# Kernel optimization log

Measured on AMD Instinct MI355X. Metric: run time of the kernel, lower is better.

The kernel has to match this reference:

```python
import jax, jax.numpy as jnp
import numpy as np

N_NODES = 50000
N_EDGES = 400000
LAT = 128
NODE_F = 3
EDGE_F = 4
OUT = 3
STEPS = 5
EPS = 1e-5


def _ln_mlp(h, w1, b1, w2, b2, g, be):
    # Linear -> ReLU -> Linear -> ReLU -> LayerNorm
    h = jax.nn.relu(h @ w1 + b1)
    h = jax.nn.relu(h @ w2 + b2)
    mu = jnp.mean(h, axis=-1, keepdims=True)
    var = jnp.mean((h - mu) ** 2, axis=-1, keepdims=True)
    return (h - mu) * jax.lax.rsqrt(var + EPS) * g + be


def _mlp_p(key, din, d):
    k = jax.random.split(key, 2)
    s1 = 1.0 / np.sqrt(din)
    s2 = 1.0 / np.sqrt(d)
    return (jax.random.normal(k[0], (din, d), jnp.float32) * s1, jnp.zeros((d,), jnp.float32),
            jax.random.normal(k[1], (d, d), jnp.float32) * s2, jnp.zeros((d,), jnp.float32),
            jnp.ones((d,), jnp.float32), jnp.zeros((d,), jnp.float32))


def setup_inputs() -> dict:
    key = jax.random.key(0)
    ks = jax.random.split(key, 8)
    d = {
        "x": jax.random.normal(ks[0], (N_NODES, NODE_F), jnp.float32),
        "edge_attr": jax.random.normal(ks[1], (N_EDGES, EDGE_F), jnp.float32),
        "edge_index": jax.random.randint(ks[2], (2, N_EDGES), 0, N_NODES, jnp.int64 if jax.config.jax_enable_x64 else jnp.int32),
    }
    for pre, din, k in (("ne", NODE_F, ks[3]), ("ee", EDGE_F, ks[4]), ("em", 3 * LAT, ks[5]), ("nm", 2 * LAT, ks[6])):
        w1, b1, w2, b2, g, be = _mlp_p(k, din, LAT)
        d[pre + "_w1"] = w1; d[pre + "_b1"] = b1
        d[pre + "_w2"] = w2; d[pre + "_b2"] = b2
        d[pre + "_g"] = g; d[pre + "_be"] = be
    kd = jax.random.split(ks[7], 2)
    d["dec_w1"] = jax.random.normal(kd[0], (LAT, LAT), jnp.float32) / np.sqrt(LAT)
    d["dec_b1"] = jnp.zeros((LAT,), jnp.float32)
    d["dec_w2"] = jax.random.normal(kd[1], (LAT, OUT), jnp.float32) / np.sqrt(LAT)
    d["dec_b2"] = jnp.zeros((OUT,), jnp.float32)
    return d


def reference(x, edge_attr, edge_index,
              ne_w1, ne_b1, ne_w2, ne_b2, ne_g, ne_be,
              ee_w1, ee_b1, ee_w2, ee_b2, ee_g, ee_be,
              em_w1, em_b1, em_w2, em_b2, em_g, em_be,
              nm_w1, nm_b1, nm_w2, nm_b2, nm_g, nm_be,
              dec_w1, dec_b1, dec_w2, dec_b2):
    n = x.shape[0]
    src, dst = edge_index[0], edge_index[1]  # PyG: edge_index[0]=source(j), [1]=target(i)

    h = _ln_mlp(x, ne_w1, ne_b1, ne_w2, ne_b2, ne_g, ne_be)          # [N, LAT]
    e = _ln_mlp(edge_attr, ee_w1, ee_b1, ee_w2, ee_b2, ee_g, ee_be)   # [E, LAT]

    for _ in range(STEPS):  # shared-weight GraphNetBlock applied STEPS times
        # message: cat([x_i, x_j, e]) = cat([h[dst], h[src], e]), aggregated at dst
        msg = _ln_mlp(jnp.concatenate([h[dst], h[src], e], axis=-1),
                      em_w1, em_b1, em_w2, em_b2, em_g, em_be)
        agg = jax.ops.segment_sum(msg, dst, num_segments=n)           # [N, LAT]
        h_new = _ln_mlp(jnp.concatenate([agg, h], axis=-1),
                        nm_w1, nm_b1, nm_w2, nm_b2, nm_g, nm_be) + h
        # new edge features use cat([x[row], x[col], e]) = cat([h[src], h[dst], e])
        e = _ln_mlp(jnp.concatenate([h[src], h[dst], e], axis=-1),
                    em_w1, em_b1, em_w2, em_b2, em_g, em_be) + e
        h = h_new

    return jax.nn.relu(h @ dec_w1 + dec_b1) @ dec_w2 + dec_b2         # [N, OUT]
```

## Files before the change

### kernel.cpp

```cpp
#include <hip/hip_runtime.h>

#define LAT 128
#define LATP 132
#define EPS 1e-5f
#define EB 32
#define TS 136

typedef __attribute__((ext_vector_type(8))) short bs8;
typedef __attribute__((ext_vector_type(4))) float fx4;

__device__ __forceinline__ float bf2f(unsigned int u) {
    return __uint_as_float(u << 16);
}
__device__ __forceinline__ unsigned short f2bf(float f) {
    unsigned int x = __float_as_uint(f);
    x += 0x7fffu + ((x >> 16) & 1u);
    return (unsigned short)(x >> 16);
}
__device__ __forceinline__ void unpack8(uint4 u, float* v) {
    v[0] = bf2f(u.x & 0xffffu); v[1] = bf2f(u.x >> 16);
    v[2] = bf2f(u.y & 0xffffu); v[3] = bf2f(u.y >> 16);
    v[4] = bf2f(u.z & 0xffffu); v[5] = bf2f(u.z >> 16);
    v[6] = bf2f(u.w & 0xffffu); v[7] = bf2f(u.w >> 16);
}
__device__ __forceinline__ uint4 pack8(const float* v) {
    uint4 u;
    u.x = (unsigned)f2bf(v[0]) | ((unsigned)f2bf(v[1]) << 16);
    u.y = (unsigned)f2bf(v[2]) | ((unsigned)f2bf(v[3]) << 16);
    u.z = (unsigned)f2bf(v[4]) | ((unsigned)f2bf(v[5]) << 16);
    u.w = (unsigned)f2bf(v[6]) | ((unsigned)f2bf(v[7]) << 16);
    return u;
}
__device__ __forceinline__ bs8 cvt8(const float* p) {
    bs8 r;
    #pragma unroll
    for (int i = 0; i < 8; i++) r[i] = (short)f2bf(p[i]);
    return r;
}

__global__ __launch_bounds__(256) void zero_kernel(float4* __restrict__ p, int n4) {
    int i = blockIdx.x * 256 + threadIdx.x;
    if (i < n4) p[i] = make_float4(0.f, 0.f, 0.f, 0.f);
}

__global__ void probe_kernel(int* __restrict__ rowtab, int* __restrict__ coltab) {
    int l = threadIdx.x;
    bs8 idv, ones;
    unsigned short ridb = f2bf((float)(l & 15));
    unsigned short oneb = f2bf(1.f);
    #pragma unroll
    for (int i = 0; i < 8; i++) { idv[i] = (short)ridb; ones[i] = (short)oneb; }
    fx4 dR = {0.f, 0.f, 0.f, 0.f};
    fx4 dC = {0.f, 0.f, 0.f, 0.f};
    dR = __builtin_amdgcn_mfma_f32_16x16x32_bf16(idv, ones, dR, 0, 0, 0);
    dC = __builtin_amdgcn_mfma_f32_16x16x32_bf16(ones, idv, dC, 0, 0, 0);
    #pragma unroll
    for (int reg = 0; reg < 4; reg++) {
        rowtab[l * 4 + reg] = ((int)(dR[reg] * (1.f / 32.f) + 0.5f)) & 15;
        coltab[l * 4 + reg] = ((int)(dC[reg] * (1.f / 32.f) + 0.5f)) & 15;
    }
}

__global__ __launch_bounds__(256) void pack_w_kernel(
    const float* __restrict__ src, unsigned short* __restrict__ dst, int KS)
{
    int id = blockIdx.x * 256 + threadIdx.x;
    if (id >= KS * 4096) return;
    int j = id & 7;
    int l = (id >> 3) & 63;
    int rest = id >> 9;
    int ks = rest % KS, nt = rest / KS;
    int k = ks * 32 + (l >> 4) * 8 + j;
    int n = nt * 16 + (l & 15);
    dst[id] = f2bf(src[k * 128 + n]);
}

template<int KIN>
__global__ __launch_bounds__(256) void encode_kernel(
    const float* __restrict__ x, unsigned short* __restrict__ out,
    const float* __restrict__ w1, const float* __restrict__ b1,
    const float* __restrict__ w2, const float* __restrict__ b2,
    const float* __restrict__ gam, const float* __restrict__ bet, int M)
{
    __shared__ float l1[8][LAT];
    __shared__ float l2[8][LAT];
    const int t = threadIdx.x;
    const int base = blockIdx.x * 8;
    const int j = t & 127, g = t >> 7;

    float wv[KIN];
    #pragma unroll
    for (int u = 0; u < KIN; u++) wv[u] = w1[u * LAT + j];
    const float bb = b1[j];
    #pragma unroll
    for (int i = 0; i < 4; i++) {
        int e = g + 2 * i; int row = base + e;
        float acc = bb;
        if (row < M) {
            #pragma unroll
            for (int u = 0; u < KIN; u++) acc += x[(size_t)row * KIN + u] * wv[u];
        }
        l1[e][j] = fmaxf(acc, 0.f);
    }
    __syncthreads();

    float s2[4] = {0.f, 0.f, 0.f, 0.f};
    for (int k = 0; k < LAT; k += 4) {
        float w[4];
        #pragma unroll
        for (int u = 0; u < 4; u++) w[u] = w2[(k + u) * LAT + j];
        #pragma unroll
        for (int i = 0; i < 4; i++) {
            int e = g + 2 * i;
            float4 v4 = *(const float4*)&l1[e][k];
            s2[i] += v4.x * w[0] + v4.y * w[1] + v4.z * w[2] + v4.w * w[3];
        }
    }
    const float b2v = b2[j];
    #pragma unroll
    for (int i = 0; i < 4; i++) { int e = g + 2 * i; l2[e][j] = fmaxf(s2[i] + b2v, 0.f); }
    __syncthreads();

    const int wv_ = t >> 6, lane = t & 63;
    #pragma unroll
    for (int which = 0; which < 2; which++) {
        int e = 2 * wv_ + which; int row = base + e;
        if (row >= M) continue;
        float v0 = l2[e][lane], v1 = l2[e][lane + 64];
        float s1 = v0 + v1, sq = v0 * v0 + v1 * v1;
        #pragma unroll
        for (int m = 32; m >= 1; m >>= 1) { s1 += __shfl_xor(s1, m); sq += __shfl_xor(sq, m); }
        float mu = s1 * (1.f / LAT);
        float var = sq * (1.f / LAT) - mu * mu;
        float inv = rsqrtf(var + EPS);
        out[(size_t)row * LAT + lane]      = f2bf((v0 - mu) * inv * gam[lane]      + bet[lane]);
        out[(size_t)row * LAT + lane + 64] = f2bf((v1 - mu) * inv * gam[lane + 64] + bet[lane + 64]);
    }
}

__global__ __launch_bounds__(256, 3) void edge_step_hybrid(
    const unsigned short* __restrict__ h, unsigned short* __restrict__ e_buf,
    float* __restrict__ agg, const int* __restrict__ ei,
    const unsigned short* __restrict__ w1p, const unsigned short* __restrict__ w2p,
    const float* __restrict__ b1, const float* __restrict__ b2,
    const float* __restrict__ gam, const float* __restrict__ bet,
    const int* __restrict__ rowtab, const int* __restrict__ coltab, int E)
{
    __shared__ __align__(16) unsigned short hd[EB * TS];
    __shared__ __align__(16) unsigned short hs[EB * TS];
    __shared__ float l1m[EB][LATP];
    __shared__ float l1n[EB][LATP];
    __shared__ int sd[EB], ss[EB];

    const int t = threadIdx.x;
    const int base = blockIdx.x * EB;
    if (t < EB) {
        int ge = base + t;
        sd[t] = (ge < E) ? ei[E + ge] : 0;
        ss[t] = (ge < E) ? ei[ge] : 0;
    }
    __syncthreads();

    for (int idx = t; idx < 2 * EB * 16; idx += 256) {
        int seg = idx / (EB * 16);
        int rem = idx - seg * (EB * 16);
        int r = rem >> 4, c = rem & 15;
        int ge = base + r;
        uint4 v = make_uint4(0, 0, 0, 0);
        if (ge < E) {
            const unsigned short* src = h + (size_t)(seg == 0 ? sd[r] : ss[r]) * LAT;
            v = *(const uint4*)(src + c * 8);
        }
        unsigned short* dstT = (seg == 0) ? hd : hs;
        *(uint4*)&dstT[r * TS + c * 8] = v;
    }
    __syncthreads();

    const int wid = t >> 6, lane = t & 63;
    const int r15 = lane & 15, q = lane >> 4;

    int4 rt = *(const int4*)(rowtab + lane * 4);
    int4 ct = *(const int4*)(coltab + lane * 4);
    int rl4[4] = {rt.x, rt.y, rt.z, rt.w};
    int cl4[4] = {ct.x, ct.y, ct.z, ct.w};

    fx4 accm[2][2], accn[2][2];
    #pragma unroll
    for (int mt = 0; mt < 2; mt++)
        #pragma unroll
        for (int nt = 0; nt < 2; nt++) { fx4 z = {0.f, 0.f, 0.f, 0.f}; accm[mt][nt] = z; }

    #pragma unroll
    for (int kc = 0; kc < 4; kc++) {
        int ks = 8 + kc;
        bs8 bf0 = *(const bs8*)(w1p + (((size_t)(wid * 2 + 0) * 12 + ks) * 64 + lane) * 8);
        bs8 bf1 = *(const bs8*)(w1p + (((size_t)(wid * 2 + 1) * 12 + ks) * 64 + lane) * 8);
        #pragma unroll
        for (int mt = 0; mt < 2; mt++) {
            bs8 ae = *(const bs8*)(e_buf + (size_t)(base + mt * 16 + r15) * LAT + kc * 32 + q * 8);
            accm[mt][0] = __builtin_amdgcn_mfma_f32_16x16x32_bf16(ae, bf0, accm[mt][0], 0, 0, 0);
            accm[mt][1] = __builtin_amdgcn_mfma_f32_16x16x32_bf16(ae, bf1, accm[mt][1], 0, 0, 0);
        }
    }
    #pragma unroll
    for (int mt = 0; mt < 2; mt++) { accn[mt][0] = accm[mt][0]; accn[mt][1] = accm[mt][1]; }

    #pragma unroll
    for (int ts = 0; ts < 2; ts++) {
        const unsigned short* tA = ts ? hs : hd;
        const unsigned short* tB = ts ? hd : hs;
        #pragma unroll
        for (int kc = 0; kc < 4; kc++) {
            int ks = ts * 4 + kc;
            bs8 bf0 = *(const bs8*)(w1p + (((size_t)(wid * 2 + 0) * 12 + ks) * 64 + lane) * 8);
            bs8 bf1 = *(const bs8*)(w1p + (((size_t)(wid * 2 + 1) * 12 + ks) * 64 + lane) * 8);
            #pragma unroll
            for (int mt = 0; mt < 2; mt++) {
                int aoff = (mt * 16 + r15) * TS + kc * 32 + q * 8;
                bs8 am = *(const bs8*)(tA + aoff);
                bs8 an = *(const bs8*)(tB + aoff);
                accm[mt][0] = __builtin_amdgcn_mfma_f32_16x16x32_bf16(am, bf0, accm[mt][0], 0, 0, 0);
                accm[mt][1] = __builtin_amdgcn_mfma_f32_16x16x32_bf16(am, bf1, accm[mt][1], 0, 0, 0);
                accn[mt][0] = __builtin_amdgcn_mfma_f32_16x16x32_bf16(an, bf0, accn[mt][0], 0, 0, 0);
                accn[mt][1] = __builtin_amdgcn_mfma_f32_16x16x32_bf16(an, bf1, accn[mt][1], 0, 0, 0);
            }
        }
    }

    #pragma unroll
    for (int nt = 0; nt < 2; nt++) {
        #pragma unroll
        for (int reg = 0; reg < 4; reg++) {
            int cg = (wid * 2 + nt) * 16 + cl4[reg];
            float bv = b1[cg];
            #pragma unroll
            for (int mt = 0; mt < 2; mt++) {
                int row = mt * 16 + rl4[reg];
                l1m[row][cg] = fmaxf(accm[mt][nt][reg] + bv, 0.f);
                l1n[row][cg] = fmaxf(accn[mt][nt][reg] + bv, 0.f);
            }
        }
    }
    __syncthreads();

    fx4 a2m[2][2], a2n[2][2];
    #pragma unroll
    for (int mt = 0; mt < 2; mt++)
        #pragma unroll
        for (int nt = 0; nt < 2; nt++) { fx4 z = {0.f, 0.f, 0.f, 0.f}; a2m[mt][nt] = z; a2n[mt][nt] = z; }

    #pragma unroll
    for (int kc = 0; kc < 4; kc++) {
        bs8 bf0 = *(const bs8*)(w2p + (((size_t)(wid * 2 + 0) * 4 + kc) * 64 + lane) * 8);
        bs8 bf1 = *(const bs8*)(w2p + (((size_t)(wid * 2 + 1) * 4 + kc) * 64 + lane) * 8);
        #pragma unroll
        for (int mt = 0; mt < 2; mt++) {
            int row = mt * 16 + r15;
            int k0 = kc * 32 + q * 8;
            bs8 am = cvt8(&l1m[row][k0]);
            bs8 an = cvt8(&l1n[row][k0]);
            a2m[mt][0] = __builtin_amdgcn_mfma_f32_16x16x32_bf16(am, bf0, a2m[mt][0], 0, 0, 0);
            a2m[mt][1] = __builtin_amdgcn_mfma_f32_16x16x32_bf16(am, bf1, a2m[mt][1], 0, 0, 0);
            a2n[mt][0] = __builtin_amdgcn_mfma_f32_16x16x32_bf16(an, bf0, a2n[mt][0], 0, 0, 0);
            a2n[mt][1] = __builtin_amdgcn_mfma_f32_16x16x32_bf16(an, bf1, a2n[mt][1], 0, 0, 0);
        }
    }
    __syncthreads();

    #pragma unroll
    for (int nt = 0; nt < 2; nt++) {
        #pragma unroll
        for (int reg = 0; reg < 4; reg++) {
            int cg = (wid * 2 + nt) * 16 + cl4[reg];
            float bv = b2[cg];
            #pragma unroll
            for (int mt = 0; mt < 2; mt++) {
                int row = mt * 16 + rl4[reg];
                l1m[row][cg] = fmaxf(a2m[mt][nt][reg] + bv, 0.f);
                l1n[row][cg] = fmaxf(a2n[mt][nt][reg] + bv, 0.f);
            }
        }
    }
    __syncthreads();

    const float g0 = gam[lane], g1 = gam[lane + 64];
    const float be0 = bet[lane], be1 = bet[lane + 64];
    #pragma unroll
    for (int which = 0; which < 8; which++) {
        int row = wid * 8 + which;
        int ge = base + row;
        float v0 = l1m[row][lane], v1 = l1m[row][lane + 64];
        float u0 = l1n[row][lane], u1 = l1n[row][lane + 64];
        float s1m = v0 + v1, sqm = v0 * v0 + v1 * v1;
        float s1n = u0 + u1, sqn = u0 * u0 + u1 * u1;
        #pragma unroll
        for (int m = 32; m >= 1; m >>= 1) {
            s1m += __shfl_xor(s1m, m); sqm += __shfl_xor(sqm, m);
            s1n += __shfl_xor(s1n, m); sqn += __shfl_xor(sqn, m);
        }
        float mum = s1m * (1.f / LAT), varm = sqm * (1.f / LAT) - mum * mum;
        float mun = s1n * (1.f / LAT), varn = sqn * (1.f / LAT) - mun * mun;
        float im = rsqrtf(varm + EPS), in_ = rsqrtf(varn + EPS);
        if (ge < E) {
            int dn = sd[row];
            atomicAdd(&agg[(size_t)dn * LAT + lane],      (v0 - mum) * im * g0 + be0);
            atomicAdd(&agg[(size_t)dn * LAT + lane + 64], (v1 - mum) * im * g1 + be1);
            float e0 = bf2f(e_buf[(size_t)ge * LAT + lane]);
            float e1 = bf2f(e_buf[(size_t)ge * LAT + lane + 64]);
            e_buf[(size_t)ge * LAT + lane]      = f2bf((u0 - mun) * in_ * g0 + be0 + e0);
            e_buf[(size_t)ge * LAT + lane + 64] = f2bf((u1 - mun) * in_ * g1 + be1 + e1);
        }
    }
}

__global__ __launch_bounds__(256, 4) void node_step_hybrid(
    float* __restrict__ agg, const unsigned short* __restrict__ h,
    unsigned short* __restrict__ h_out,
    const unsigned short* __restrict__ w1p, const unsigned short* __restrict__ w2p,
    const float* __restrict__ b1, const float* __restrict__ b2,
    const float* __restrict__ gam, const float* __restrict__ bet,
    const int* __restrict__ rowtab, const int* __restrict__ coltab, int N)
{
    __shared__ __align__(16) unsigned short aT[EB * TS];
    __shared__ __align__(16) unsigned short hT[EB * TS];
    __shared__ float l1f[EB][LATP];

    const int t = threadIdx.x;
    const int base = blockIdx.x * EB;

    for (int idx = t; idx < EB * 16; idx += 256) {
        int r = idx >> 4, c = idx & 15;
        int n = base + r;
        if (n < N) {
            float* ap = agg + (size_t)n * LAT + c * 8;
            float4 f0 = *(float4*)ap;
            float4 f1 = *(float4*)(ap + 4);
            float av[8] = {f0.x, f0.y, f0.z, f0.w, f1.x, f1.y, f1.z, f1.w};
            *(uint4*)&aT[r * TS + c * 8] = pack8(av);
            *(float4*)ap = make_float4(0.f, 0.f, 0.f, 0.f);
            *(float4*)(ap + 4) = make_float4(0.f, 0.f, 0.f, 0.f);
            *(uint4*)&hT[r * TS + c * 8] = *(const uint4*)(h + (size_t)n * LAT + c * 8);
        } else {
            uint4 z = make_uint4(0, 0, 0, 0);
            *(uint4*)&aT[r * TS + c * 8] = z;
            *(uint4*)&hT[r * TS + c * 8] = z;
        }
    }
    __syncthreads();

    const int wid = t >> 6, lane = t & 63;
    const int r15 = lane & 15, q = lane >> 4;

    int4 rt = *(const int4*)(rowtab + lane * 4);
    int4 ct = *(const int4*)(coltab + lane * 4);
    int rl4[4] = {rt.x, rt.y, rt.z, rt.w};
    int cl4[4] = {ct.x, ct.y, ct.z, ct.w};

    fx4 acc[2][2];
    #pragma unroll
    for (int mt = 0; mt < 2; mt++)
        #pragma unroll
        for (int nt = 0; nt < 2; nt++) { fx4 z = {0.f, 0.f, 0.f, 0.f}; acc[mt][nt] = z; }

    #pragma unroll
    for (int ts = 0; ts < 2; ts++) {
        const unsigned short* tA = ts ? hT : aT;
        #pragma unroll
        for (int kc = 0; kc < 4; kc++) {
            int ks = ts * 4 + kc;
            bs8 bf0 = *(const bs8*)(w1p + (((size_t)(wid * 2 + 0) * 8 + ks) * 64 + lane) * 8);
            bs8 bf1 = *(const bs8*)(w1p + (((size_t)(wid * 2 + 1) * 8 + ks) * 64 + lane) * 8);
            #pragma unroll
            for (int mt = 0; mt < 2; mt++) {
                bs8 a = *(const bs8*)(tA + (mt * 16 + r15) * TS + kc * 32 + q * 8);
                acc[mt][0] = __builtin_amdgcn_mfma_f32_16x16x32_bf16(a, bf0, acc[mt][0], 0, 0, 0);
                acc[mt][1] = __builtin_amdgcn_mfma_f32_16x16x32_bf16(a, bf1, acc[mt][1], 0, 0, 0);
            }
        }
    }
    #pragma unroll
    for (int nt = 0; nt < 2; nt++) {
        #pragma unroll
        for (int reg = 0; reg < 4; reg++) {
            int cg = (wid * 2 + nt) * 16 + cl4[reg];
            float bv = b1[cg];
            #pragma unroll
            for (int mt = 0; mt < 2; mt++) {
                int row = mt * 16 + rl4[reg];
                l1f[row][cg] = fmaxf(acc[mt][nt][reg] + bv, 0.f);
            }
        }
    }
    __syncthreads();

    fx4 a2[2][2];
    #pragma unroll
    for (int mt = 0; mt < 2; mt++)
        #pragma unroll
        for (int nt = 0; nt < 2; nt++) { fx4 z = {0.f, 0.f, 0.f, 0.f}; a2[mt][nt] = z; }

    #pragma unroll
    for (int kc = 0; kc < 4; kc++) {
        bs8 bf0 = *(const bs8*)(w2p + (((size_t)(wid * 2 + 0) * 4 + kc) * 64 + lane) * 8);
        bs8 bf1 = *(const bs8*)(w2p + (((size_t)(wid * 2 + 1) * 4 + kc) * 64 + lane) * 8);
        #pragma unroll
        for (int mt = 0; mt < 2; mt++) {
            int row = mt * 16 + r15;
            int k0 = kc * 32 + q * 8;
            bs8 a = cvt8(&l1f[row][k0]);
            a2[mt][0] = __builtin_amdgcn_mfma_f32_16x16x32_bf16(a, bf0, a2[mt][0], 0, 0, 0);
            a2[mt][1] = __builtin_amdgcn_mfma_f32_16x16x32_bf16(a, bf1, a2[mt][1], 0, 0, 0);
        }
    }
    __syncthreads();

    #pragma unroll
    for (int nt = 0; nt < 2; nt++) {
        #pragma unroll
        for (int reg = 0; reg < 4; reg++) {
            int cg = (wid * 2 + nt) * 16 + cl4[reg];
            float bv = b2[cg];
            #pragma unroll
            for (int mt = 0; mt < 2; mt++) {
                int row = mt * 16 + rl4[reg];
                l1f[row][cg] = fmaxf(a2[mt][nt][reg] + bv, 0.f);
            }
        }
    }
    __syncthreads();

    const float g0 = gam[lane], g1 = gam[lane + 64];
    const float be0 = bet[lane], be1 = bet[lane + 64];
    #pragma unroll
    for (int which = 0; which < 8; which++) {
        int row = wid * 8 + which;
        int n = base + row;
        float v0 = l1f[row][lane], v1 = l1f[row][lane + 64];
        float s1 = v0 + v1, sq = v0 * v0 + v1 * v1;
        #pragma unroll
        for (int m = 32; m >= 1; m >>= 1) { s1 += __shfl_xor(s1, m); sq += __shfl_xor(sq, m); }
        float mu = s1 * (1.f / LAT);
        float var = sq * (1.f / LAT) - mu * mu;
        float inv = rsqrtf(var + EPS);
        if (n < N) {
            float h0 = bf2f(hT[row * TS + lane]);
            float h1 = bf2f(hT[row * TS + lane + 64]);
            h_out[(size_t)n * LAT + lane]      = f2bf((v0 - mu) * inv * g0 + be0 + h0);
            h_out[(size_t)n * LAT + lane + 64] = f2bf((v1 - mu) * inv * g1 + be1 + h1);
        }
    }
}

__global__ __launch_bounds__(256) void decode_kernel(
    const unsigned short* __restrict__ h, float* __restrict__ out,
    const float* __restrict__ w1, const float* __restrict__ b1,
    const float* __restrict__ w2, const float* __restrict__ b2, int N)
{
    __shared__ float hv[8][LAT], d1[8][LAT];
    const int t = threadIdx.x;
    const int base = blockIdx.x * 8;
    for (int idx = t; idx < 8 * 16; idx += 256) {
        int e = idx >> 4; int c8 = (idx & 15) * 8;
        int n = base + e;
        float v[8];
        for (int u = 0; u < 8; u++) v[u] = 0.f;
        if (n < N) unpack8(*(const uint4*)(h + (size_t)n * LAT + c8), v);
        for (int u = 0; u < 8; u++) hv[e][c8 + u] = v[u];
    }
    __syncthreads();
    const int j = t & 127, g = t >> 7;
    float s[4] = {0, 0, 0, 0};
    for (int k = 0; k < LAT; k += 4) {
        float w[4];
        #pragma unroll
        for (int u = 0; u < 4; u++) w[u] = w1[(k + u) * LAT + j];
        #pragma unroll
        for (int i = 0; i < 4; i++) {
            int e = g + 2 * i;
            float4 v4 = *(const float4*)&hv[e][k];
            s[i] += v4.x * w[0] + v4.y * w[1] + v4.z * w[2] + v4.w * w[3];
        }
    }
    const float bb = b1[j];
    #pragma unroll
    for (int i = 0; i < 4; i++) { int e = g + 2 * i; d1[e][j] = fmaxf(s[i] + bb, 0.f); }
    __syncthreads();
    const int wv_ = t >> 6, lane = t & 63;
    #pragma unroll
    for (int which = 0; which < 2; which++) {
        int e = 2 * wv_ + which; int n = base + e;
        if (n >= N) continue;
        float a0 = 0.f, a1 = 0.f, a2 = 0.f;
        #pragma unroll
        for (int kk = 0; kk < 2; kk++) {
            int k = lane + 64 * kk;
            float v = d1[e][k];
            a0 += v * w2[k * 3 + 0];
            a1 += v * w2[k * 3 + 1];
            a2 += v * w2[k * 3 + 2];
        }
        #pragma unroll
        for (int m = 32; m >= 1; m >>= 1) {
            a0 += __shfl_xor(a0, m); a1 += __shfl_xor(a1, m); a2 += __shfl_xor(a2, m);
        }
        if (lane == 0) {
            out[(size_t)n * 3 + 0] = a0 + b2[0];
            out[(size_t)n * 3 + 1] = a1 + b2[1];
            out[(size_t)n * 3 + 2] = a2 + b2[2];
        }
    }
}

extern "C" void kernel_launch(void* const* d_in, const int* in_sizes, int n_in,
                              void* d_out, int out_size, void* d_ws, size_t ws_size,
                              hipStream_t stream) {
    const float* x         = (const float*)d_in[0];
    const float* edge_attr = (const float*)d_in[1];
    const int*   ei        = (const int*)d_in[2];
    const float* ne_w1 = (const float*)d_in[3];  const float* ne_b1 = (const float*)d_in[4];
    const float* ne_w2 = (const float*)d_in[5];  const float* ne_b2 = (const float*)d_in[6];
    const float* ne_g  = (const float*)d_in[7];  const float* ne_be = (const float*)d_in[8];
    const float* ee_w1 = (const float*)d_in[9];  const float* ee_b1 = (const float*)d_in[10];
    const float* ee_w2 = (const float*)d_in[11]; const float* ee_b2 = (const float*)d_in[12];
    const float* ee_g  = (const float*)d_in[13]; const float* ee_be = (const float*)d_in[14];
    const float* em_w1 = (const float*)d_in[15]; const float* em_b1 = (const float*)d_in[16];
    const float* em_w2 = (const float*)d_in[17]; const float* em_b2 = (const float*)d_in[18];
    const float* em_g  = (const float*)d_in[19]; const float* em_be = (const float*)d_in[20];
    const float* nm_w1 = (const float*)d_in[21]; const float* nm_b1 = (const float*)d_in[22];
    const float* nm_w2 = (const float*)d_in[23]; const float* nm_b2 = (const float*)d_in[24];
    const float* nm_g  = (const float*)d_in[25]; const float* nm_be = (const float*)d_in[26];
    const float* dec_w1 = (const float*)d_in[27]; const float* dec_b1 = (const float*)d_in[28];
    const float* dec_w2 = (const float*)d_in[29]; const float* dec_b2 = (const float*)d_in[30];

    const int N = in_sizes[0] / 3;
    const int E = in_sizes[2] / 2;

    unsigned short* hA   = (unsigned short*)d_ws;
    unsigned short* hB   = hA + (size_t)N * LAT;
    unsigned short* ebuf = hB + (size_t)N * LAT;
    float*          agg  = (float*)(ebuf + (size_t)E * LAT);
    unsigned short* ew1p = (unsigned short*)(agg + (size_t)N * LAT);
    unsigned short* ew2p = ew1p + 12 * 4096;
    unsigned short* nw1p = ew2p + 4 * 4096;
    unsigned short* nw2p = nw1p + 8 * 4096;
    int*            rowtab = (int*)(nw2p + 4 * 4096);
    int*            coltab = rowtab + 256;

    const dim3 blk(256);

    probe_kernel<<<1, 64, 0, stream>>>(rowtab, coltab);
    pack_w_kernel<<<(12 * 4096 + 255) / 256, blk, 0, stream>>>(em_w1, ew1p, 12);
    pack_w_kernel<<<(4  * 4096 + 255) / 256, blk, 0, stream>>>(em_w2, ew2p, 4);
    pack_w_kernel<<<(8  * 4096 + 255) / 256, blk, 0, stream>>>(nm_w1, nw1p, 8);
    pack_w_kernel<<<(4  * 4096 + 255) / 256, blk, 0, stream>>>(nm_w2, nw2p, 4);

    const int n4 = (N * LAT) / 4;
    zero_kernel<<<(n4 + 255) / 256, blk, 0, stream>>>((float4*)agg, n4);

    const int nb_n8 = (N + 7) / 8;
    const int nb_e8 = (E + 7) / 8;
    encode_kernel<3><<<nb_n8, blk, 0, stream>>>(x, hA, ne_w1, ne_b1, ne_w2, ne_b2, ne_g, ne_be, N);
    encode_kernel<4><<<nb_e8, blk, 0, stream>>>(edge_attr, ebuf, ee_w1, ee_b1, ee_w2, ee_b2, ee_g, ee_be, E);

    const int nb_e32 = (E + EB - 1) / EB;
    const int nb_n32 = (N + EB - 1) / EB;
    unsigned short* hc = hA; unsigned short* hn = hB;
    for (int s = 0; s < 5; s++) {
        edge_step_hybrid<<<nb_e32, blk, 0, stream>>>(hc, ebuf, agg, ei,
                                                     ew1p, ew2p, em_b1, em_b2, em_g, em_be,
                                                     rowtab, coltab, E);
        node_step_hybrid<<<nb_n32, blk, 0, stream>>>(agg, hc, hn,
                                                     nw1p, nw2p, nm_b1, nm_b2, nm_g, nm_be,
                                                     rowtab, coltab, N);
        unsigned short* tmp = hc; hc = hn; hn = tmp;
    }
    decode_kernel<<<nb_n8, blk, 0, stream>>>(hc, (float*)d_out, dec_w1, dec_b1, dec_w2, dec_b2, N);
}
```

Measured before the change: 1.992 ms.

## Use bf16 MFMA in encoders and alias edge-step shared memory for occupancy

The node and edge encoders now compute their second linear layer with bf16 MFMA on pre-packed weights over 32-row tiles, instead of scalar fp32 FMAs over 8-row tiles. The edge step kernel aliases the gathered h tiles and the layer-1 activation buffers into one shared pool, with an added barrier, and raises launch bounds to 4 blocks per SM. The aim is to cut encoder compute and lift edge-step occupancy. In exchange, the encoder's second layer is rounded to bf16 and the edge step gains an extra sync.

```diff
diff --git a/kernel.cpp b/kernel.cpp
--- a/kernel.cpp
+++ b/kernel.cpp
@@ -76,16 +76,17 @@
 }
 
 template<int KIN>
-__global__ __launch_bounds__(256) void encode_kernel(
+__global__ __launch_bounds__(256, 4) void encode_hybrid(
     const float* __restrict__ x, unsigned short* __restrict__ out,
     const float* __restrict__ w1, const float* __restrict__ b1,
-    const float* __restrict__ w2, const float* __restrict__ b2,
-    const float* __restrict__ gam, const float* __restrict__ bet, int M)
+    const unsigned short* __restrict__ w2p, const float* __restrict__ b2,
+    const float* __restrict__ gam, const float* __restrict__ bet,
+    const int* __restrict__ rowtab, const int* __restrict__ coltab, int M)
 {
-    __shared__ float l1[8][LAT];
-    __shared__ float l2[8][LAT];
+    __shared__ float l1f[EB][LATP];
+
     const int t = threadIdx.x;
-    const int base = blockIdx.x * 8;
+    const int base = blockIdx.x * EB;
     const int j = t & 127, g = t >> 7;
 
     float wv[KIN];
@@ -93,52 +94,82 @@
     for (int u = 0; u < KIN; u++) wv[u] = w1[u * LAT + j];
     const float bb = b1[j];
     #pragma unroll
-    for (int i = 0; i < 4; i++) {
-        int e = g + 2 * i; int row = base + e;
+    for (int i = 0; i < 16; i++) {
+        int r = g + 2 * i; int row = base + r;
         float acc = bb;
         if (row < M) {
             #pragma unroll
             for (int u = 0; u < KIN; u++) acc += x[(size_t)row * KIN + u] * wv[u];
         }
-        l1[e][j] = fmaxf(acc, 0.f);
-    }
-    __syncthreads();
-
-    float s2[4] = {0.f, 0.f, 0.f, 0.f};
-    for (int k = 0; k < LAT; k += 4) {
-        float w[4];
-        #pragma unroll
-        for (int u = 0; u < 4; u++) w[u] = w2[(k + u) * LAT + j];
-        #pragma unroll
-        for (int i = 0; i < 4; i++) {
-            int e = g + 2 * i;
-            float4 v4 = *(const float4*)&l1[e][k];
-            s2[i] += v4.x * w[0] + v4.y * w[1] + v4.z * w[2] + v4.w * w[3];
-        }
-    }
-    const float b2v = b2[j];
-    #pragma unroll
-    for (int i = 0; i < 4; i++) { int e = g + 2 * i; l2[e][j] = fmaxf(s2[i] + b2v, 0.f); }
-    __syncthreads();
-
-    const int wv_ = t >> 6, lane = t & 63;
-    #pragma unroll
-    for (int which = 0; which < 2; which++) {
-        int e = 2 * wv_ + which; int row = base + e;
-        if (row >= M) continue;
-        float v0 = l2[e][lane], v1 = l2[e][lane + 64];
+        l1f[r][j] = fmaxf(acc, 0.f);
+    }
+    __syncthreads();
+
+    const int wid = t >> 6, lane = t & 63;
+    const int r15 = lane & 15, q = lane >> 4;
+
+    int4 rt = *(const int4*)(rowtab + lane * 4);
+    int4 ct = *(const int4*)(coltab + lane * 4);
+    int rl4[4] = {rt.x, rt.y, rt.z, rt.w};
+    int cl4[4] = {ct.x, ct.y, ct.z, ct.w};
+
+    fx4 a2[2][2];
+    #pragma unroll
+    for (int mt = 0; mt < 2; mt++)
+        #pragma unroll
+        for (int nt = 0; nt < 2; nt++) { fx4 z = {0.f, 0.f, 0.f, 0.f}; a2[mt][nt] = z; }
+
+    #pragma unroll
+    for (int kc = 0; kc < 4; kc++) {
+        bs8 bf0 = *(const bs8*)(w2p + (((size_t)(wid * 2 + 0) * 4 + kc) * 64 + lane) * 8);
+        bs8 bf1 = *(const bs8*)(w2p + (((size_t)(wid * 2 + 1) * 4 + kc) * 64 + lane) * 8);
+        #pragma unroll
+        for (int mt = 0; mt < 2; mt++) {
+            int row = mt * 16 + r15;
+            int k0 = kc * 32 + q * 8;
+            bs8 a = cvt8(&l1f[row][k0]);
+            a2[mt][0] = __builtin_amdgcn_mfma_f32_16x16x32_bf16(a, bf0, a2[mt][0], 0, 0, 0);
+            a2[mt][1] = __builtin_amdgcn_mfma_f32_16x16x32_bf16(a, bf1, a2[mt][1], 0, 0, 0);
+        }
+    }
+    __syncthreads();
+
+    #pragma unroll
+    for (int nt = 0; nt < 2; nt++) {
+        #pragma unroll
+        for (int reg = 0; reg < 4; reg++) {
+            int cg = (wid * 2 + nt) * 16 + cl4[reg];
+            float bv = b2[cg];
+            #pragma unroll
+            for (int mt = 0; mt < 2; mt++) {
+                int row = mt * 16 + rl4[reg];
+                l1f[row][cg] = fmaxf(a2[mt][nt][reg] + bv, 0.f);
+            }
+        }
+    }
+    __syncthreads();
+
+    const float g0 = gam[lane], g1 = gam[lane + 64];
+    const float be0 = bet[lane], be1 = bet[lane + 64];
+    #pragma unroll
+    for (int which = 0; which < 8; which++) {
+        int row = wid * 8 + which;
+        int rowg = base + row;
+        float v0 = l1f[row][lane], v1 = l1f[row][lane + 64];
         float s1 = v0 + v1, sq = v0 * v0 + v1 * v1;
         #pragma unroll
         for (int m = 32; m >= 1; m >>= 1) { s1 += __shfl_xor(s1, m); sq += __shfl_xor(sq, m); }
         float mu = s1 * (1.f / LAT);
         float var = sq * (1.f / LAT) - mu * mu;
         float inv = rsqrtf(var + EPS);
-        out[(size_t)row * LAT + lane]      = f2bf((v0 - mu) * inv * gam[lane]      + bet[lane]);
-        out[(size_t)row * LAT + lane + 64] = f2bf((v1 - mu) * inv * gam[lane + 64] + bet[lane + 64]);
-    }
-}
-
-__global__ __launch_bounds__(256, 3) void edge_step_hybrid(
+        if (rowg < M) {
+            out[(size_t)rowg * LAT + lane]      = f2bf((v0 - mu) * inv * g0 + be0);
+            out[(size_t)rowg * LAT + lane + 64] = f2bf((v1 - mu) * inv * g1 + be1);
+        }
+    }
+}
+
+__global__ __launch_bounds__(256, 4) void edge_step_hybrid(
     const unsigned short* __restrict__ h, unsigned short* __restrict__ e_buf,
     float* __restrict__ agg, const int* __restrict__ ei,
     const unsigned short* __restrict__ w1p, const unsigned short* __restrict__ w2p,
@@ -146,11 +177,12 @@
     const float* __restrict__ gam, const float* __restrict__ bet,
     const int* __restrict__ rowtab, const int* __restrict__ coltab, int E)
 {
-    __shared__ __align__(16) unsigned short hd[EB * TS];
-    __shared__ __align__(16) unsigned short hs[EB * TS];
-    __shared__ float l1m[EB][LATP];
-    __shared__ float l1n[EB][LATP];
+    __shared__ __align__(16) float poolf[2 * EB * LATP];
     __shared__ int sd[EB], ss[EB];
+    unsigned short* hd = (unsigned short*)poolf;
+    unsigned short* hs = (unsigned short*)poolf + EB * TS;
+    float (*l1m)[LATP] = (float(*)[LATP])poolf;
+    float (*l1n)[LATP] = (float(*)[LATP])(poolf + EB * LATP);
 
     const int t = threadIdx.x;
     const int base = blockIdx.x * EB;
@@ -226,6 +258,7 @@
             }
         }
     }
+    __syncthreads();
 
     #pragma unroll
     for (int nt = 0; nt < 2; nt++) {
@@ -543,7 +576,9 @@
     unsigned short* ew2p = ew1p + 12 * 4096;
     unsigned short* nw1p = ew2p + 4 * 4096;
     unsigned short* nw2p = nw1p + 8 * 4096;
-    int*            rowtab = (int*)(nw2p + 4 * 4096);
+    unsigned short* neW2p = nw2p + 4 * 4096;
+    unsigned short* eeW2p = neW2p + 4 * 4096;
+    int*            rowtab = (int*)(eeW2p + 4 * 4096);
     int*            coltab = rowtab + 256;
 
     const dim3 blk(256);
@@ -553,17 +588,19 @@
     pack_w_kernel<<<(4  * 4096 + 255) / 256, blk, 0, stream>>>(em_w2, ew2p, 4);
     pack_w_kernel<<<(8  * 4096 + 255) / 256, blk, 0, stream>>>(nm_w1, nw1p, 8);
     pack_w_kernel<<<(4  * 4096 + 255) / 256, blk, 0, stream>>>(nm_w2, nw2p, 4);
+    pack_w_kernel<<<(4  * 4096 + 255) / 256, blk, 0, stream>>>(ne_w2, neW2p, 4);
+    pack_w_kernel<<<(4  * 4096 + 255) / 256, blk, 0, stream>>>(ee_w2, eeW2p, 4);
 
     const int n4 = (N * LAT) / 4;
     zero_kernel<<<(n4 + 255) / 256, blk, 0, stream>>>((float4*)agg, n4);
 
-    const int nb_n8 = (N + 7) / 8;
-    const int nb_e8 = (E + 7) / 8;
-    encode_kernel<3><<<nb_n8, blk, 0, stream>>>(x, hA, ne_w1, ne_b1, ne_w2, ne_b2, ne_g, ne_be, N);
-    encode_kernel<4><<<nb_e8, blk, 0, stream>>>(edge_attr, ebuf, ee_w1, ee_b1, ee_w2, ee_b2, ee_g, ee_be, E);
-
+    const int nb_n32 = (N + EB - 1) / EB;
     const int nb_e32 = (E + EB - 1) / EB;
-    const int nb_n32 = (N + EB - 1) / EB;
+    encode_hybrid<3><<<nb_n32, blk, 0, stream>>>(x, hA, ne_w1, ne_b1, neW2p, ne_b2,
+                                                 ne_g, ne_be, rowtab, coltab, N);
+    encode_hybrid<4><<<nb_e32, blk, 0, stream>>>(edge_attr, ebuf, ee_w1, ee_b1, eeW2p, ee_b2,
+                                                 ee_g, ee_be, rowtab, coltab, E);
+
     unsigned short* hc = hA; unsigned short* hn = hB;
     for (int s = 0; s < 5; s++) {
         edge_step_hybrid<<<nb_e32, blk, 0, stream>>>(hc, ebuf, agg, ei,
@@ -574,5 +611,6 @@
                                                      rowtab, coltab, N);
         unsigned short* tmp = hc; hc = hn; hn = tmp;
     }
+    const int nb_n8 = (N + 7) / 8;
     decode_kernel<<<nb_n8, blk, 0, stream>>>(hc, (float*)d_out, dec_w1, dec_b1, dec_w2, dec_b2, N);
 }
```

Measured after the change: 1.633 ms (median of 4 runs). -18.0%, faster.
